# Performance work log

Hardware: AMD Instinct MI355X
Metric: run time of the kernel (lower is better)

Reference implementation:

```python
import jax, jax.numpy as jnp
import numpy as np

B, S, D, H = 2, 2048, 1024, 16
HD = D // H
SCALE = 1.0 / np.sqrt(HD)


def setup_inputs() -> dict:
    key = jax.random.key(0)
    ks = jax.random.split(key, 12)
    def xavier(k, shape):
        fan_in, fan_out = shape[1], shape[0]
        lim = np.sqrt(6.0 / (fan_in + fan_out))
        return jax.random.uniform(k, shape, jnp.float32, -lim, lim)
    return {
        "query": jax.random.normal(ks[0], (B, S, D), jnp.float32),
        "key": jax.random.normal(ks[1], (B, S, D), jnp.float32),
        "value": jax.random.normal(ks[2], (B, S, D), jnp.float32),
        "attention_mask": jax.random.randint(ks[3], (B, 1, 1, S), 0, 2, jnp.int32),
        "wq": xavier(ks[4], (D, D)), "bq": jnp.zeros((D,), jnp.float32),
        "wk": xavier(ks[5], (D, D)), "bk": jnp.zeros((D,), jnp.float32),
        "wv": xavier(ks[6], (D, D)), "bv": jnp.zeros((D,), jnp.float32),
        "wo": xavier(ks[7], (D, D)), "bo": jnp.zeros((D,), jnp.float32),
    }


def reference(query, key, value, attention_mask, wq, bq, wk, bk, wv, bv, wo, bo):
    # nn.Linear: x @ W^T + b
    def split_heads(x):
        return x.reshape(B, S, H, HD).transpose(0, 2, 1, 3)  # [B,H,S,HD]
    Q = split_heads(query @ wq.T + bq)
    K = split_heads(key @ wk.T + bk)
    V = split_heads(value @ wv.T + bv)
    scores = jnp.einsum("bhqd,bhkd->bhqk", Q, K) * SCALE  # [B,H,S,S]
    scores = jnp.where(attention_mask == 0, jnp.float32(-1e9), scores)
    attn = jax.nn.softmax(scores, axis=-1)
    ctx = jnp.einsum("bhqk,bhkd->bhqd", attn, V)
    ctx = ctx.transpose(0, 2, 1, 3).reshape(B, S, D)
    out = ctx @ wo.T + bo
    return out, attn
```

## Files before the change

kernel.cpp:

```cpp
#include <hip/hip_runtime.h>
#include <hip/hip_bf16.h>
#include <cstddef>

#define Bn 2
#define Sn 2048
#define Dn 1024
#define Hn 16
#define HDn 64
static constexpr float SCALE_ = 0.125f;

typedef __attribute__((ext_vector_type(8))) short short8;
typedef __attribute__((ext_vector_type(4))) float f4;

__device__ inline f4 mfma16(short8 a, short8 b, f4 c) {
  return __builtin_amdgcn_mfma_f32_16x16x32_bf16(a, b, c, 0, 0, 0);
}

typedef const __attribute__((address_space(1))) void gv_t;
typedef __attribute__((address_space(3))) void lv_t;
__device__ inline void gload_lds16(const void* g, void* l) {
  __builtin_amdgcn_global_load_lds((gv_t*)g, (lv_t*)l, 16, 0, 0);
}

struct CvtArgs { const float* src[6]; __bf16* dst[6]; int n[6]; };

__global__ __launch_bounds__(256) void cvt_bf16(CvtArgs a) {
  const int z = blockIdx.y;
  const float* __restrict__ s = a.src[z];
  __bf16* __restrict__ d = a.dst[z];
  const int n = a.n[z];
  for (int i = (blockIdx.x * 256 + threadIdx.x) * 8; i < n; i += gridDim.x * 256 * 8) {
    f4 x = *(const f4*)(s + i);
    f4 y = *(const f4*)(s + i + 4);
    __bf16 t[8] __attribute__((aligned(16)));
    t[0] = (__bf16)x.x; t[1] = (__bf16)x.y; t[2] = (__bf16)x.z; t[3] = (__bf16)x.w;
    t[4] = (__bf16)y.x; t[5] = (__bf16)y.y; t[6] = (__bf16)y.z; t[7] = (__bf16)y.w;
    *(short8*)(d + i) = *(short8*)t;
  }
}

struct GemmPtrs { const __bf16* A[2]; const __bf16* W[2]; const float* bias[2]; void* C[2]; };

template<int MODE>
__global__ __launch_bounds__(256) void gemm128(GemmPtrs P, int M, int N, int K) {
  __shared__ __bf16 As[128 * 32];
  __shared__ __bf16 Bs[128 * 32];
  const int z = blockIdx.z;
  const __bf16* __restrict__ A = P.A[z];
  const __bf16* __restrict__ W = P.W[z];
  const float* __restrict__ bias = P.bias[z];
  const int tid = threadIdx.x, wid = tid >> 6, lane = tid & 63;
  const int m0 = blockIdx.y * 128, n0 = blockIdx.x * 128;
  const int wm = (wid >> 1) * 64, wn = (wid & 1) * 64;
  const int lr = lane & 15, lg = lane >> 4;
  const int srow = lane >> 2, scol = (lane & 3) * 8;
  f4 acc[4][4] = {};
  for (int k0 = 0; k0 < K; k0 += 32) {
    #pragma unroll
    for (int c = 0; c < 2; c++) {
      const int chunk = wid * 2 + c;
      gload_lds16(A + (size_t)(m0 + chunk * 16 + srow) * K + k0 + scol, &As[chunk * 512]);
      gload_lds16(W + (size_t)(n0 + chunk * 16 + srow) * K + k0 + scol, &Bs[chunk * 512]);
    }
    __syncthreads();
    short8 af[4], bfr[4];
    #pragma unroll
    for (int i = 0; i < 4; i++) af[i]  = *(const short8*)&As[(wm + i * 16 + lr) * 32 + lg * 8];
    #pragma unroll
    for (int j = 0; j < 4; j++) bfr[j] = *(const short8*)&Bs[(wn + j * 16 + lr) * 32 + lg * 8];
    #pragma unroll
    for (int i = 0; i < 4; i++)
      #pragma unroll
      for (int j = 0; j < 4; j++) acc[i][j] = mfma16(af[i], bfr[j], acc[i][j]);
    __syncthreads();
  }
  #pragma unroll
  for (int i = 0; i < 4; i++) {
    #pragma unroll
    for (int j = 0; j < 4; j++) {
      const int row = m0 + wm + i * 16 + lg * 4;
      const int col = n0 + wn + j * 16 + lr;
      const float bb = bias[col];
      if (MODE == 2) {
        __bf16 o[4] __attribute__((aligned(8)));
        #pragma unroll
        for (int r = 0; r < 4; r++) o[r] = (__bf16)(acc[i][j][r] + bb);
        __bf16* dst = (__bf16*)P.C[z] + ((size_t)(row >> 11) * Dn + col) * Sn + (row & 2047);
        *(ulong1*)dst = *(ulong1*)o;
      } else {
        #pragma unroll
        for (int r = 0; r < 4; r++) {
          float v = acc[i][j][r] + bb;
          if (MODE == 0) ((__bf16*)P.C[z])[(size_t)(row + r) * N + col] = (__bf16)v;
          else           ((float*)P.C[z])[(size_t)(row + r) * N + col] = v;
        }
      }
    }
  }
}

__global__ __launch_bounds__(256, 4) void attn_kernel(
    const __bf16* __restrict__ Q, const __bf16* __restrict__ Kb,
    const __bf16* __restrict__ Vt, const int* __restrict__ mask,
    float* __restrict__ attn_out, __bf16* __restrict__ ctx)
{
  __shared__ __bf16 stg[4][16][40];
  __shared__ float red[4][16][64];
  __shared__ float sums[4][16];
  __shared__ float finals[16];

  const int b = blockIdx.z, h = blockIdx.y, q0 = blockIdx.x * 16;
  const int tid = threadIdx.x, wid = tid >> 6, lane = tid & 63;
  const int lr = lane & 15, lg = lane >> 4;

  const __bf16* Qbase = Q + ((size_t)(b * Sn + q0)) * Dn + h * HDn;
  const short8 qf0 = *(const short8*)(Qbase + (size_t)lr * Dn + lg * 8);
  const short8 qf1 = *(const short8*)(Qbase + (size_t)lr * Dn + 32 + lg * 8);

  const __bf16* Kbase = Kb + (size_t)b * Sn * Dn + h * HDn;
  const int* mrow = mask + b * Sn;

  float s[4] = {0.f, 0.f, 0.f, 0.f};
  unsigned mbits = 0;
  #pragma unroll 4
  for (int ct = 0; ct < 32; ct++) {
    const int col0 = wid * 512 + ct * 16;
    const __bf16* Kp = Kbase + (size_t)(col0 + lr) * Dn + lg * 8;
    const short8 kf0 = *(const short8*)Kp;
    const short8 kf1 = *(const short8*)(Kp + 32);
    f4 a = {0.f, 0.f, 0.f, 0.f};
    a = mfma16(qf0, kf0, a);
    a = mfma16(qf1, kf1, a);
    const bool mk = mrow[col0 + lr] != 0;
    mbits |= (mk ? 1u : 0u) << ct;
    #pragma unroll
    for (int r = 0; r < 4; r++) s[r] += mk ? __expf(a[r] * SCALE_) : 0.f;
  }
  #pragma unroll
  for (int d = 1; d < 16; d <<= 1)
    #pragma unroll
    for (int r = 0; r < 4; r++) s[r] += __shfl_xor(s[r], d);
  if (lr == 0) {
    #pragma unroll
    for (int r = 0; r < 4; r++) sums[wid][lg * 4 + r] = s[r];
  }
  __syncthreads();
  if (tid < 16) {
    float t = sums[0][tid] + sums[1][tid] + sums[2][tid] + sums[3][tid];
    finals[tid] = 1.0f / fmaxf(t, 1e-30f);
  }
  __syncthreads();
  float inv[4];
  #pragma unroll
  for (int r = 0; r < 4; r++) inv[r] = finals[lg * 4 + r];

  f4 pacc[4] = {{0.f,0.f,0.f,0.f},{0.f,0.f,0.f,0.f},{0.f,0.f,0.f,0.f},{0.f,0.f,0.f,0.f}};
  const __bf16* Vtb = Vt + ((size_t)(b * Hn + h)) * HDn * Sn;
  float* arow = attn_out + (((size_t)(b * Hn + h)) * Sn + q0 + lg * 4) * Sn;
  #pragma unroll 2
  for (int ct2 = 0; ct2 < 16; ct2++) {
    const int col0 = wid * 512 + ct2 * 32;
    #pragma unroll
    for (int t = 0; t < 2; t++) {
      const int colt = col0 + t * 16;
      const __bf16* Kp = Kbase + (size_t)(colt + lr) * Dn + lg * 8;
      const short8 kf0 = *(const short8*)Kp;
      const short8 kf1 = *(const short8*)(Kp + 32);
      f4 a = {0.f, 0.f, 0.f, 0.f};
      a = mfma16(qf0, kf0, a);
      a = mfma16(qf1, kf1, a);
      const bool mk = (mbits >> (ct2 * 2 + t)) & 1u;
      #pragma unroll
      for (int r = 0; r < 4; r++) {
        const float p = mk ? __expf(a[r] * SCALE_) * inv[r] : 0.f;
        arow[(size_t)r * Sn + colt + lr] = p;
        stg[wid][lg * 4 + r][t * 16 + lr] = (__bf16)p;
      }
    }
    const short8 af = *(const short8*)&stg[wid][lr][lg * 8];
    #pragma unroll
    for (int nt = 0; nt < 4; nt++) {
      const short8 bfr = *(const short8*)(Vtb + (size_t)(nt * 16 + lr) * Sn + col0 + lg * 8);
      pacc[nt] = mfma16(af, bfr, pacc[nt]);
    }
  }
  __syncthreads();

  #pragma unroll
  for (int nt = 0; nt < 4; nt++)
    #pragma unroll
    for (int r = 0; r < 4; r++)
      red[wid][lg * 4 + r][nt * 16 + lr] = pacc[nt][r];
  __syncthreads();
  const int q = tid >> 4, c0 = (tid & 15) * 4;
  __bf16* crow = ctx + ((size_t)(b * Sn + q0 + q)) * Dn + h * HDn + c0;
  __bf16 o[4] __attribute__((aligned(8)));
  #pragma unroll
  for (int j = 0; j < 4; j++) {
    float v = red[0][q][c0 + j] + red[1][q][c0 + j] + red[2][q][c0 + j] + red[3][q][c0 + j];
    o[j] = (__bf16)v;
  }
  *(ulong1*)crow = *(ulong1*)o;
}

extern "C" void kernel_launch(void* const* d_in, const int* in_sizes, int n_in,
                              void* d_out, int out_size, void* d_ws, size_t ws_size,
                              hipStream_t stream) {
  const float* query = (const float*)d_in[0];
  const float* key   = (const float*)d_in[1];
  const float* value = (const float*)d_in[2];
  const int*   mask  = (const int*)d_in[3];
  const float* wq = (const float*)d_in[4];
  const float* bq = (const float*)d_in[5];
  const float* wk = (const float*)d_in[6];
  const float* bk = (const float*)d_in[7];
  const float* wv = (const float*)d_in[8];
  const float* bv = (const float*)d_in[9];
  const float* wo = (const float*)d_in[10];
  const float* bo = (const float*)d_in[11];

  float* out  = (float*)d_out;
  float* attn = out + (size_t)Bn * Sn * Dn;

  const size_t NA = (size_t)4194304;
  const size_t NW = (size_t)1048576;
  __bf16* A0  = (__bf16*)d_ws;
  __bf16* A1  = A0 + NA;
  __bf16* Wbf = A1 + NA;
  __bf16* Qb  = Wbf + 4 * NW;
  __bf16* Kbf = Qb + NA;
  __bf16* ctxb = A0;
  __bf16* Vtb  = A1;

  CvtArgs c6;
  c6.src[0] = wq;    c6.dst[0] = Wbf;          c6.n[0] = (int)NW;
  c6.src[1] = wk;    c6.dst[1] = Wbf + NW;     c6.n[1] = (int)NW;
  c6.src[2] = wv;    c6.dst[2] = Wbf + 2 * NW; c6.n[2] = (int)NW;
  c6.src[3] = wo;    c6.dst[3] = Wbf + 3 * NW; c6.n[3] = (int)NW;
  c6.src[4] = query; c6.dst[4] = A0;           c6.n[4] = (int)NA;
  c6.src[5] = key;   c6.dst[5] = A1;           c6.n[5] = (int)NA;
  cvt_bf16<<<dim3(256, 6), 256, 0, stream>>>(c6);

  GemmPtrs gqk;
  gqk.A[0] = A0; gqk.W[0] = Wbf;      gqk.bias[0] = bq; gqk.C[0] = Qb;
  gqk.A[1] = A1; gqk.W[1] = Wbf + NW; gqk.bias[1] = bk; gqk.C[1] = Kbf;
  gemm128<0><<<dim3(8, 32, 2), 256, 0, stream>>>(gqk, 4096, 1024, 1024);

  CvtArgs c1;
  c1.src[0] = value; c1.dst[0] = A0; c1.n[0] = (int)NA;
  for (int i = 1; i < 6; i++) { c1.src[i] = value; c1.dst[i] = A0; c1.n[i] = 0; }
  cvt_bf16<<<dim3(256, 1), 256, 0, stream>>>(c1);

  GemmPtrs gv;
  gv.A[0] = A0; gv.W[0] = Wbf + 2 * NW; gv.bias[0] = bv; gv.C[0] = Vtb;
  gv.A[1] = gv.A[0]; gv.W[1] = gv.W[0]; gv.bias[1] = gv.bias[0]; gv.C[1] = gv.C[0];
  gemm128<2><<<dim3(8, 32, 1), 256, 0, stream>>>(gv, 4096, 1024, 1024);

  attn_kernel<<<dim3(128, 16, 2), 256, 0, stream>>>(Qb, Kbf, Vtb, mask, attn, ctxb);

  GemmPtrs go;
  go.A[0] = ctxb; go.W[0] = Wbf + 3 * NW; go.bias[0] = bo; go.C[0] = out;
  go.A[1] = go.A[0]; go.W[1] = go.W[0]; go.bias[1] = go.bias[0]; go.C[1] = go.C[0];
  gemm128<1><<<dim3(8, 32, 1), 256, 0, stream>>>(go, 4096, 1024, 1024);
}
```

Measured before the change: 976.4 us.

## Cache attention probabilities in registers and batch QKV projections into one launch

New measurement: 997.9 us. +2.2%, slower.

```diff
diff --git a/kernel.cpp b/kernel.cpp
--- a/kernel.cpp
+++ b/kernel.cpp
@@ -22,7 +22,16 @@
   __builtin_amdgcn_global_load_lds((gv_t*)g, (lv_t*)l, 16, 0, 0);
 }
 
-struct CvtArgs { const float* src[6]; __bf16* dst[6]; int n[6]; };
+__device__ inline unsigned packbf2(float x, float y) {
+  __bf16 a = (__bf16)x, b = (__bf16)y;
+  unsigned short ua = __builtin_bit_cast(unsigned short, a);
+  unsigned short ub = __builtin_bit_cast(unsigned short, b);
+  return (unsigned)ua | ((unsigned)ub << 16);
+}
+__device__ inline float unp_lo(unsigned u) { return __builtin_bit_cast(float, u << 16); }
+__device__ inline float unp_hi(unsigned u) { return __builtin_bit_cast(float, u & 0xffff0000u); }
+
+struct CvtArgs { const float* src[7]; __bf16* dst[7]; int n[7]; };
 
 __global__ __launch_bounds__(256) void cvt_bf16(CvtArgs a) {
   const int z = blockIdx.y;
@@ -39,9 +48,9 @@
   }
 }
 
-struct GemmPtrs { const __bf16* A[2]; const __bf16* W[2]; const float* bias[2]; void* C[2]; };
-
-template<int MODE>
+struct GemmPtrs { const __bf16* A[3]; const __bf16* W[3]; const float* bias[3];
+                  void* C[3]; int mode[3]; };
+
 __global__ __launch_bounds__(256) void gemm128(GemmPtrs P, int M, int N, int K) {
   __shared__ __bf16 As[128 * 32];
   __shared__ __bf16 Bs[128 * 32];
@@ -49,6 +58,7 @@
   const __bf16* __restrict__ A = P.A[z];
   const __bf16* __restrict__ W = P.W[z];
   const float* __restrict__ bias = P.bias[z];
+  const int mode = P.mode[z];
   const int tid = threadIdx.x, wid = tid >> 6, lane = tid & 63;
   const int m0 = blockIdx.y * 128, n0 = blockIdx.x * 128;
   const int wm = (wid >> 1) * 64, wn = (wid & 1) * 64;
@@ -81,25 +91,26 @@
       const int row = m0 + wm + i * 16 + lg * 4;
       const int col = n0 + wn + j * 16 + lr;
       const float bb = bias[col];
-      if (MODE == 2) {
+      if (mode == 2) {
         __bf16 o[4] __attribute__((aligned(8)));
         #pragma unroll
         for (int r = 0; r < 4; r++) o[r] = (__bf16)(acc[i][j][r] + bb);
         __bf16* dst = (__bf16*)P.C[z] + ((size_t)(row >> 11) * Dn + col) * Sn + (row & 2047);
         *(ulong1*)dst = *(ulong1*)o;
+      } else if (mode == 0) {
+        #pragma unroll
+        for (int r = 0; r < 4; r++)
+          ((__bf16*)P.C[z])[(size_t)(row + r) * N + col] = (__bf16)(acc[i][j][r] + bb);
       } else {
         #pragma unroll
-        for (int r = 0; r < 4; r++) {
-          float v = acc[i][j][r] + bb;
-          if (MODE == 0) ((__bf16*)P.C[z])[(size_t)(row + r) * N + col] = (__bf16)v;
-          else           ((float*)P.C[z])[(size_t)(row + r) * N + col] = v;
-        }
+        for (int r = 0; r < 4; r++)
+          ((float*)P.C[z])[(size_t)(row + r) * N + col] = acc[i][j][r] + bb;
       }
     }
   }
 }
 
-__global__ __launch_bounds__(256, 4) void attn_kernel(
+__global__ __launch_bounds__(256) void attn_kernel(
     const __bf16* __restrict__ Q, const __bf16* __restrict__ Kb,
     const __bf16* __restrict__ Vt, const int* __restrict__ mask,
     float* __restrict__ attn_out, __bf16* __restrict__ ctx)
@@ -120,69 +131,60 @@
   const __bf16* Kbase = Kb + (size_t)b * Sn * Dn + h * HDn;
   const int* mrow = mask + b * Sn;
 
-  float s[4] = {0.f, 0.f, 0.f, 0.f};
-  unsigned mbits = 0;
-  #pragma unroll 4
+  float ssum = 0.f;
+  unsigned pr[64];
+  #pragma unroll
   for (int ct = 0; ct < 32; ct++) {
     const int col0 = wid * 512 + ct * 16;
     const __bf16* Kp = Kbase + (size_t)(col0 + lr) * Dn + lg * 8;
     const short8 kf0 = *(const short8*)Kp;
     const short8 kf1 = *(const short8*)(Kp + 32);
     f4 a = {0.f, 0.f, 0.f, 0.f};
-    a = mfma16(qf0, kf0, a);
-    a = mfma16(qf1, kf1, a);
-    const bool mk = mrow[col0 + lr] != 0;
-    mbits |= (mk ? 1u : 0u) << ct;
-    #pragma unroll
-    for (int r = 0; r < 4; r++) s[r] += mk ? __expf(a[r] * SCALE_) : 0.f;
-  }
-  #pragma unroll
-  for (int d = 1; d < 16; d <<= 1)
-    #pragma unroll
-    for (int r = 0; r < 4; r++) s[r] += __shfl_xor(s[r], d);
-  if (lr == 0) {
-    #pragma unroll
-    for (int r = 0; r < 4; r++) sums[wid][lg * 4 + r] = s[r];
-  }
+    a = mfma16(kf0, qf0, a);
+    a = mfma16(kf1, qf1, a);
+    const int4 m4 = *(const int4*)&mrow[col0 + lg * 4];
+    float p0 = m4.x ? __expf(a[0] * SCALE_) : 0.f;
+    float p1 = m4.y ? __expf(a[1] * SCALE_) : 0.f;
+    float p2 = m4.z ? __expf(a[2] * SCALE_) : 0.f;
+    float p3 = m4.w ? __expf(a[3] * SCALE_) : 0.f;
+    ssum += (p0 + p1) + (p2 + p3);
+    pr[2 * ct]     = packbf2(p0, p1);
+    pr[2 * ct + 1] = packbf2(p2, p3);
+  }
+
+  ssum += __shfl_xor(ssum, 16);
+  ssum += __shfl_xor(ssum, 32);
+  if (lane < 16) sums[wid][lane] = ssum;
   __syncthreads();
   if (tid < 16) {
     float t = sums[0][tid] + sums[1][tid] + sums[2][tid] + sums[3][tid];
     finals[tid] = 1.0f / fmaxf(t, 1e-30f);
   }
   __syncthreads();
-  float inv[4];
-  #pragma unroll
-  for (int r = 0; r < 4; r++) inv[r] = finals[lg * 4 + r];
+  const float invq = finals[lr];
 
   f4 pacc[4] = {{0.f,0.f,0.f,0.f},{0.f,0.f,0.f,0.f},{0.f,0.f,0.f,0.f},{0.f,0.f,0.f,0.f}};
   const __bf16* Vtb = Vt + ((size_t)(b * Hn + h)) * HDn * Sn;
-  float* arow = attn_out + (((size_t)(b * Hn + h)) * Sn + q0 + lg * 4) * Sn;
-  #pragma unroll 2
-  for (int ct2 = 0; ct2 < 16; ct2++) {
-    const int col0 = wid * 512 + ct2 * 32;
-    #pragma unroll
-    for (int t = 0; t < 2; t++) {
-      const int colt = col0 + t * 16;
-      const __bf16* Kp = Kbase + (size_t)(colt + lr) * Dn + lg * 8;
-      const short8 kf0 = *(const short8*)Kp;
-      const short8 kf1 = *(const short8*)(Kp + 32);
-      f4 a = {0.f, 0.f, 0.f, 0.f};
-      a = mfma16(qf0, kf0, a);
-      a = mfma16(qf1, kf1, a);
-      const bool mk = (mbits >> (ct2 * 2 + t)) & 1u;
-      #pragma unroll
-      for (int r = 0; r < 4; r++) {
-        const float p = mk ? __expf(a[r] * SCALE_) * inv[r] : 0.f;
-        arow[(size_t)r * Sn + colt + lr] = p;
-        stg[wid][lg * 4 + r][t * 16 + lr] = (__bf16)p;
-      }
-    }
+  float* arow = attn_out + (((size_t)(b * Hn + h)) * Sn + q0 + lr) * Sn;
+  #pragma unroll
+  for (int c = 0; c < 16; c++) {
+    const int cols0 = wid * 512 + c * 32;
+    uint2 w0 = make_uint2(pr[4 * c], pr[4 * c + 1]);
+    uint2 w1 = make_uint2(pr[4 * c + 2], pr[4 * c + 3]);
+    *(uint2*)&stg[wid][lr][lg * 4]      = w0;
+    *(uint2*)&stg[wid][lr][16 + lg * 4] = w1;
     const short8 af = *(const short8*)&stg[wid][lr][lg * 8];
     #pragma unroll
     for (int nt = 0; nt < 4; nt++) {
-      const short8 bfr = *(const short8*)(Vtb + (size_t)(nt * 16 + lr) * Sn + col0 + lg * 8);
+      const short8 bfr = *(const short8*)(Vtb + (size_t)(nt * 16 + lr) * Sn + cols0 + lg * 8);
       pacc[nt] = mfma16(af, bfr, pacc[nt]);
     }
+    f4 v0 = { unp_lo(pr[4*c]) * invq,   unp_hi(pr[4*c]) * invq,
+              unp_lo(pr[4*c+1]) * invq, unp_hi(pr[4*c+1]) * invq };
+    f4 v1 = { unp_lo(pr[4*c+2]) * invq, unp_hi(pr[4*c+2]) * invq,
+              unp_lo(pr[4*c+3]) * invq, unp_hi(pr[4*c+3]) * invq };
+    *(f4*)&arow[cols0 + lg * 4]      = v0;
+    *(f4*)&arow[cols0 + 16 + lg * 4] = v1;
   }
   __syncthreads();
 
@@ -190,7 +192,7 @@
   for (int nt = 0; nt < 4; nt++)
     #pragma unroll
     for (int r = 0; r < 4; r++)
-      red[wid][lg * 4 + r][nt * 16 + lr] = pacc[nt][r];
+      red[wid][lg * 4 + r][nt * 16 + lr] = pacc[nt][r] * finals[lg * 4 + r];
   __syncthreads();
   const int q = tid >> 4, c0 = (tid & 15) * 4;
   __bf16* crow = ctx + ((size_t)(b * Sn + q0 + q)) * Dn + h * HDn + c0;
@@ -224,42 +226,36 @@
 
   const size_t NA = (size_t)4194304;
   const size_t NW = (size_t)1048576;
-  __bf16* A0  = (__bf16*)d_ws;
-  __bf16* A1  = A0 + NA;
-  __bf16* Wbf = A1 + NA;
-  __bf16* Qb  = Wbf + 4 * NW;
-  __bf16* Kbf = Qb + NA;
-  __bf16* ctxb = A0;
-  __bf16* Vtb  = A1;
-
-  CvtArgs c6;
-  c6.src[0] = wq;    c6.dst[0] = Wbf;          c6.n[0] = (int)NW;
-  c6.src[1] = wk;    c6.dst[1] = Wbf + NW;     c6.n[1] = (int)NW;
-  c6.src[2] = wv;    c6.dst[2] = Wbf + 2 * NW; c6.n[2] = (int)NW;
-  c6.src[3] = wo;    c6.dst[3] = Wbf + 3 * NW; c6.n[3] = (int)NW;
-  c6.src[4] = query; c6.dst[4] = A0;           c6.n[4] = (int)NA;
-  c6.src[5] = key;   c6.dst[5] = A1;           c6.n[5] = (int)NA;
-  cvt_bf16<<<dim3(256, 6), 256, 0, stream>>>(c6);
-
-  GemmPtrs gqk;
-  gqk.A[0] = A0; gqk.W[0] = Wbf;      gqk.bias[0] = bq; gqk.C[0] = Qb;
-  gqk.A[1] = A1; gqk.W[1] = Wbf + NW; gqk.bias[1] = bk; gqk.C[1] = Kbf;
-  gemm128<0><<<dim3(8, 32, 2), 256, 0, stream>>>(gqk, 4096, 1024, 1024);
-
-  CvtArgs c1;
-  c1.src[0] = value; c1.dst[0] = A0; c1.n[0] = (int)NA;
-  for (int i = 1; i < 6; i++) { c1.src[i] = value; c1.dst[i] = A0; c1.n[i] = 0; }
-  cvt_bf16<<<dim3(256, 1), 256, 0, stream>>>(c1);
-
-  GemmPtrs gv;
-  gv.A[0] = A0; gv.W[0] = Wbf + 2 * NW; gv.bias[0] = bv; gv.C[0] = Vtb;
-  gv.A[1] = gv.A[0]; gv.W[1] = gv.W[0]; gv.bias[1] = gv.bias[0]; gv.C[1] = gv.C[0];
-  gemm128<2><<<dim3(8, 32, 1), 256, 0, stream>>>(gv, 4096, 1024, 1024);
+  __bf16* Wbf  = (__bf16*)d_ws;
+  __bf16* Qb   = Wbf + 4 * NW;
+  __bf16* Kbf  = Qb + NA;
+  __bf16* Vtb  = Kbf + NA;
+  __bf16* ctxb = Vtb + NA;
+  __bf16* cQ = (__bf16*)attn;
+  __bf16* cK = cQ + NA;
+  __bf16* cV = cK + NA;
+
+  CvtArgs c7;
+  c7.src[0] = wq;    c7.dst[0] = Wbf;          c7.n[0] = (int)NW;
+  c7.src[1] = wk;    c7.dst[1] = Wbf + NW;     c7.n[1] = (int)NW;
+  c7.src[2] = wv;    c7.dst[2] = Wbf + 2 * NW; c7.n[2] = (int)NW;
+  c7.src[3] = wo;    c7.dst[3] = Wbf + 3 * NW; c7.n[3] = (int)NW;
+  c7.src[4] = query; c7.dst[4] = cQ;           c7.n[4] = (int)NA;
+  c7.src[5] = key;   c7.dst[5] = cK;           c7.n[5] = (int)NA;
+  c7.src[6] = value; c7.dst[6] = cV;           c7.n[6] = (int)NA;
+  cvt_bf16<<<dim3(256, 7), 256, 0, stream>>>(c7);
+
+  GemmPtrs g3;
+  g3.A[0] = cQ; g3.W[0] = Wbf;          g3.bias[0] = bq; g3.C[0] = Qb;  g3.mode[0] = 0;
+  g3.A[1] = cK; g3.W[1] = Wbf + NW;     g3.bias[1] = bk; g3.C[1] = Kbf; g3.mode[1] = 0;
+  g3.A[2] = cV; g3.W[2] = Wbf + 2 * NW; g3.bias[2] = bv; g3.C[2] = Vtb; g3.mode[2] = 2;
+  gemm128<<<dim3(8, 32, 3), 256, 0, stream>>>(g3, 4096, 1024, 1024);
 
   attn_kernel<<<dim3(128, 16, 2), 256, 0, stream>>>(Qb, Kbf, Vtb, mask, attn, ctxb);
 
   GemmPtrs go;
-  go.A[0] = ctxb; go.W[0] = Wbf + 3 * NW; go.bias[0] = bo; go.C[0] = out;
-  go.A[1] = go.A[0]; go.W[1] = go.W[0]; go.bias[1] = go.bias[0]; go.C[1] = go.C[0];
-  gemm128<1><<<dim3(8, 32, 1), 256, 0, stream>>>(go, 4096, 1024, 1024);
-}
+  go.A[0] = ctxb; go.W[0] = Wbf + 3 * NW; go.bias[0] = bo; go.C[0] = out; go.mode[0] = 1;
+  go.A[1] = go.A[0]; go.W[1] = go.W[0]; go.bias[1] = go.bias[0]; go.C[1] = go.C[0]; go.mode[1] = 1;
+  go.A[2] = go.A[0]; go.W[2] = go.W[0]; go.bias[2] = go.bias[0]; go.C[2] = go.C[0]; go.mode[2] = 1;
+  gemm128<<<dim3(8, 32, 1), 256, 0, stream>>>(go, 4096, 1024, 1024);
+}
```
